# Kernel tuning notes

Measured on AMD Instinct MI355X. Metric: run time of the kernel, lower is better.

Reference implementation:

```python
import jax, jax.numpy as jnp
import numpy as np

EMB = 1024
HEAD = 64

def setup_inputs() -> dict:
    key = jax.random.key(0)
    k1, k2, k3, k4, k5 = jax.random.split(key, 5)
    x = jax.random.normal(k1, (4, 4096, EMB), dtype=jnp.float32)
    # qkv linear: weight [3*HEAD, EMB] torch-style -> store as [EMB, 3*HEAD]
    W_qkv = jax.random.normal(k2, (EMB, 3 * HEAD), dtype=jnp.float32) * (1.0 / np.sqrt(EMB))
    b_qkv = jax.random.normal(k3, (3 * HEAD,), dtype=jnp.float32) * 0.01
    W_out = jax.random.normal(k4, (HEAD, EMB), dtype=jnp.float32) * (1.0 / np.sqrt(HEAD))
    b_out = jax.random.normal(k5, (EMB,), dtype=jnp.float32) * 0.01
    return {"x": x, "W_qkv": W_qkv, "b_qkv": b_qkv, "W_out": W_out, "b_out": b_out}

def reference(x, W_qkv, b_qkv, W_out, b_out):
    qkv = jnp.einsum('bse,ed->bsd', x, W_qkv) + b_qkv            # [B,S,3H]
    q, k, v = jnp.split(qkv, 3, axis=-1)                          # each [B,S,H]
    scale = 1.0 / jnp.sqrt(jnp.asarray(q.shape[-1], q.dtype))
    scores = jnp.einsum('bqh,bkh->bqk', q, k) * scale             # [B,S,S]
    attn = jax.nn.softmax(scores, axis=-1)
    ctx = jnp.einsum('bqk,bkh->bqh', attn, v)                     # [B,S,H]
    return jnp.einsum('bqh,he->bqe', ctx, W_out) + b_out          # [B,S,E]
```

## Files before the change

### kernel.cpp

```cpp
#include <hip/hip_runtime.h>
#include <hip/hip_bf16.h>


#define LD 72

typedef __attribute__((ext_vector_type(8))) short short8;
typedef __attribute__((ext_vector_type(4))) short short4v;
typedef __attribute__((ext_vector_type(4))) float floatx4;

#define MFMA(a, b, c) __builtin_amdgcn_mfma_f32_16x16x32_bf16((a), (b), (c), 0, 0, 0)

__device__ __forceinline__ unsigned short f2bf(float f) {
  union { float f; unsigned u; } c; c.f = f;
  unsigned u = c.u + 0x7fffu + ((c.u >> 16) & 1u);
  return (unsigned short)(u >> 16);
}
__device__ __forceinline__ float asf(unsigned u) {
  union { unsigned u; float f; } c; c.u = u; return c.f;
}

__global__ __launch_bounds__(256) void prep_kernel(
    const float* __restrict__ Wqkv, const float* __restrict__ Wout,
    unsigned short* __restrict__ WtQkv, unsigned short* __restrict__ WtOut) {
  int idx = blockIdx.x * 256 + threadIdx.x;
  if (idx < 192 * 1024) {
    int n = idx >> 10, k = idx & 1023;
    WtQkv[idx] = f2bf(Wqkv[k * 192 + n]);
  } else if (idx < 192 * 1024 + 1024 * 64) {
    int j = idx - 192 * 1024;
    int e = j >> 6, d = j & 63;
    WtOut[j] = f2bf(Wout[d * 1024 + e]);
  }
}

__global__ __launch_bounds__(256, 2) void qkv_kernel(
    const float* __restrict__ x, const unsigned short* __restrict__ WtQkv,
    const float* __restrict__ bqkv,
    unsigned short* __restrict__ Qg, unsigned short* __restrict__ Kg,
    unsigned short* __restrict__ Vtg) {
  __shared__ __align__(16) unsigned short eQ[32 * LD];
  __shared__ __align__(16) unsigned short eK[32 * LD];
  __shared__ __align__(16) unsigned short eV[64 * 40];

  const int tid = threadIdx.x;
  const int wave = tid >> 6, lane = tid & 63, quad = lane >> 4, l16 = lane & 15;
  const int row0 = blockIdx.x * 32;
  const int colbase = wave * 48;

  floatx4 acc[2][3];
#pragma unroll
  for (int rt = 0; rt < 2; rt++)
#pragma unroll
    for (int t = 0; t < 3; t++) acc[rt][t] = (floatx4)(0.0f);

  const float* pA0 = x + (size_t)(row0 + l16) * 1024 + quad * 8;
  const float* pA1 = pA0 + 16 * 1024;
  const unsigned short* pB[3];
#pragma unroll
  for (int t = 0; t < 3; t++)
    pB[t] = WtQkv + (size_t)(colbase + t * 16 + l16) * 1024 + quad * 8;

  float4 ax[2][2][2];
  uint4 bw[3][2];
#pragma unroll
  for (int kh = 0; kh < 2; kh++) {
    ax[0][kh][0] = *(const float4*)(pA0 + kh * 32);
    ax[0][kh][1] = *(const float4*)(pA0 + kh * 32 + 4);
    ax[1][kh][0] = *(const float4*)(pA1 + kh * 32);
    ax[1][kh][1] = *(const float4*)(pA1 + kh * 32 + 4);
  }
#pragma unroll
  for (int t = 0; t < 3; t++) {
    bw[t][0] = *(const uint4*)(pB[t]);
    bw[t][1] = *(const uint4*)(pB[t] + 32);
  }

  for (int kc = 0; kc < 16; kc++) {
    short8 af[2][2];
#pragma unroll
    for (int rt = 0; rt < 2; rt++)
#pragma unroll
      for (int kh = 0; kh < 2; kh++) {
        const float* f0 = (const float*)&ax[rt][kh][0];
        const float* f1 = (const float*)&ax[rt][kh][1];
        short8 a;
        a[0] = (short)f2bf(f0[0]); a[1] = (short)f2bf(f0[1]);
        a[2] = (short)f2bf(f0[2]); a[3] = (short)f2bf(f0[3]);
        a[4] = (short)f2bf(f1[0]); a[5] = (short)f2bf(f1[1]);
        a[6] = (short)f2bf(f1[2]); a[7] = (short)f2bf(f1[3]);
        af[rt][kh] = a;
      }
    if (kc < 15) {
#pragma unroll
      for (int kh = 0; kh < 2; kh++) {
        ax[0][kh][0] = *(const float4*)(pA0 + 64 + kh * 32);
        ax[0][kh][1] = *(const float4*)(pA0 + 64 + kh * 32 + 4);
        ax[1][kh][0] = *(const float4*)(pA1 + 64 + kh * 32);
        ax[1][kh][1] = *(const float4*)(pA1 + 64 + kh * 32 + 4);
      }
    }
#pragma unroll
    for (int t = 0; t < 3; t++) {
      short8 b0 = __builtin_bit_cast(short8, bw[t][0]);
      short8 b1 = __builtin_bit_cast(short8, bw[t][1]);
      if (kc < 15) {
        bw[t][0] = *(const uint4*)(pB[t] + 64);
        bw[t][1] = *(const uint4*)(pB[t] + 96);
      }
#pragma unroll
      for (int rt = 0; rt < 2; rt++) {
        acc[rt][t] = MFMA(af[rt][0], b0, acc[rt][t]);
        acc[rt][t] = MFMA(af[rt][1], b1, acc[rt][t]);
      }
    }
    pA0 += 64; pA1 += 64;
#pragma unroll
    for (int t = 0; t < 3; t++) pB[t] += 64;
  }

  const int b = row0 >> 12, srow = row0 & 4095;
#pragma unroll
  for (int rt = 0; rt < 2; rt++)
#pragma unroll
    for (int t = 0; t < 3; t++) {
      int col = colbase + t * 16 + l16;
      float bias = bqkv[col];
      int sec = col >> 6, d = col & 63;
#pragma unroll
      for (int r = 0; r < 4; r++) {
        int lrow = rt * 16 + quad * 4 + r;
        float v = acc[rt][t][r] + bias;
        if (sec == 0)      eQ[lrow * LD + d] = f2bf(v * 0.125f);
        else if (sec == 1) eK[lrow * LD + d] = f2bf(v);
        else               eV[d * 40 + lrow] = f2bf(v);
      }
    }
  __syncthreads();
  {
    int r = tid >> 3, sg = tid & 7;
    *(uint4*)(Qg + (size_t)(row0 + r) * 64 + sg * 8) = *(const uint4*)(&eQ[r * LD + sg * 8]);
    *(uint4*)(Kg + (size_t)(row0 + r) * 64 + sg * 8) = *(const uint4*)(&eK[r * LD + sg * 8]);
    int tile = tid >> 7, rem = tid & 127, d = rem >> 1, half = rem & 1;
    *(uint4*)(Vtg + (((size_t)b * 256 + (srow >> 4) + tile) * 64 + d) * 16 + half * 8)
        = *(const uint4*)(&eV[d * 40 + tile * 16 + half * 8]);
  }
}

__global__ __launch_bounds__(256, 4) void attn_kernel(
    const unsigned short* __restrict__ Qg, const unsigned short* __restrict__ Kg,
    const unsigned short* __restrict__ Vtg,
    unsigned short* __restrict__ Opart, float* __restrict__ Lpart) {
  __shared__ __align__(16) unsigned short Ks[64 * LD];
  __shared__ __align__(16) unsigned short Vs[64 * LD];
  __shared__ __align__(16) unsigned short QP[64 * LD];

  const int tid = threadIdx.x;
  const int wave = tid >> 6, lane = tid & 63, quad = lane >> 4, l16 = lane & 15;
  const int bid = blockIdx.x;
  const int combo = bid & 15, qt = bid >> 4;
  const int b = combo >> 2, split = combo & 3;
  const int q0 = qt * 64, key0 = split * 1024;

  {
    int r = tid >> 2, seg = tid & 3;
    const uint4* s = (const uint4*)(Qg + ((size_t)b * 4096 + q0 + r) * 64 + seg * 16);
    *(uint4*)(&QP[r * LD + seg * 16])     = s[0];
    *(uint4*)(&QP[r * LD + seg * 16 + 8]) = s[1];
  }
  short8 aq0 = *(const short8*)(&QP[(wave * 16 + l16) * LD + quad * 8]);
  short8 aq1 = *(const short8*)(&QP[(wave * 16 + l16) * LD + 32 + quad * 8]);

  floatx4 o[4];
  float lsum[4];
#pragma unroll
  for (int t = 0; t < 4; t++) o[t] = (floatx4)(0.0f);
#pragma unroll
  for (int r = 0; r < 4; r++) lsum[r] = 0.0f;

  const int kr = tid >> 2, kseg = tid & 3;
  const unsigned short* Kbase = Kg + ((size_t)b * 4096 + key0) * 64;
  const unsigned short* Vt0 = Vtg + ((size_t)b * 256 + (key0 >> 4)) * 1024;

  uint4 pk0, pk1, pv0, pv1;
  pk0 = *(const uint4*)(Kbase + (size_t)kr * 64 + kseg * 16);
  pk1 = *(const uint4*)(Kbase + (size_t)kr * 64 + kseg * 16 + 8);
  pv0 = *(const uint4*)(Vt0 + ((size_t)kseg * 64 + kr) * 16);
  pv1 = *(const uint4*)(Vt0 + ((size_t)kseg * 64 + kr) * 16 + 8);

  unsigned short* Pw = &QP[wave * 16 * LD];

  for (int kc = 0; kc < 16; kc++) {
    __syncthreads();
    *(uint4*)(&Ks[kr * LD + kseg * 16])     = pk0;
    *(uint4*)(&Ks[kr * LD + kseg * 16 + 8]) = pk1;
    *(uint4*)(&Vs[kr * LD + kseg * 16])     = pv0;
    *(uint4*)(&Vs[kr * LD + kseg * 16 + 8]) = pv1;
    __syncthreads();
    if (kc < 15) {
      int nk = (kc + 1) * 64;
      int tl = (kc + 1) * 4 + kseg;
      pk0 = *(const uint4*)(Kbase + (size_t)(nk + kr) * 64 + kseg * 16);
      pk1 = *(const uint4*)(Kbase + (size_t)(nk + kr) * 64 + kseg * 16 + 8);
      pv0 = *(const uint4*)(Vt0 + ((size_t)tl * 64 + kr) * 16);
      pv1 = *(const uint4*)(Vt0 + ((size_t)tl * 64 + kr) * 16 + 8);
    }

    floatx4 sc[4];
#pragma unroll
    for (int t = 0; t < 4; t++) sc[t] = (floatx4)(0.0f);
#pragma unroll
    for (int t = 0; t < 4; t++) {
      short8 b0 = *(const short8*)(&Ks[(t * 16 + l16) * LD + quad * 8]);
      short8 b1 = *(const short8*)(&Ks[(t * 16 + l16) * LD + 32 + quad * 8]);
      sc[t] = MFMA(aq0, b0, sc[t]);
      sc[t] = MFMA(aq1, b1, sc[t]);
    }

#pragma unroll
    for (int r = 0; r < 4; r++) {
#pragma unroll
      for (int t = 0; t < 4; t++) {
        float pv = __expf(sc[t][r]);
        lsum[r] += pv;
        Pw[(quad * 4 + r) * LD + t * 16 + l16] = f2bf(pv);
      }
    }
    short8 ap0 = *(const short8*)(&Pw[l16 * LD + quad * 8]);
    short8 ap1 = *(const short8*)(&Pw[l16 * LD + 32 + quad * 8]);
#pragma unroll
    for (int t = 0; t < 4; t++) {
      short8 b0 = *(const short8*)(&Vs[(t * 16 + l16) * LD + quad * 8]);
      short8 b1 = *(const short8*)(&Vs[(t * 16 + l16) * LD + 32 + quad * 8]);
      o[t] = MFMA(ap0, b0, o[t]);
      o[t] = MFMA(ap1, b1, o[t]);
    }
  }

#pragma unroll
  for (int r = 0; r < 4; r++) {
#pragma unroll
    for (int off = 1; off < 16; off <<= 1) lsum[r] += __shfl_xor(lsum[r], off, 64);
  }

  unsigned short* Ob = Opart + ((size_t)bid * 64 + wave * 16) * 64;
#pragma unroll
  for (int t = 0; t < 4; t++)
#pragma unroll
    for (int r = 0; r < 4; r++)
      Ob[(quad * 4 + r) * 64 + t * 16 + l16] = f2bf(o[t][r]);
  if (l16 == 0) {
#pragma unroll
    for (int r = 0; r < 4; r++)
      Lpart[bid * 64 + wave * 16 + quad * 4 + r] = lsum[r];
  }
}

__global__ __launch_bounds__(256, 4) void combine_kernel(
    const unsigned short* __restrict__ Opart, const float* __restrict__ Lpart,
    const unsigned short* __restrict__ WtOut, const float* __restrict__ bout,
    float* __restrict__ out) {
  __shared__ __align__(16) unsigned short Cs[4][16 * LD];
  __shared__ __align__(16) unsigned short Wl[128 * LD];

  const int tid = threadIdx.x;
  const int wave = tid >> 6, lane = tid & 63, quad = lane >> 4, l16 = lane & 15;
  const int cid = blockIdx.x;
  const int eq = cid & 3, qt = (cid >> 2) & 63, b = cid >> 8;
  const int e0 = eq * 256;

  const int q = lane >> 2, d0 = (lane & 3) * 16;
  float accv[16];
#pragma unroll
  for (int i = 0; i < 16; i++) accv[i] = 0.0f;
  float lq = 0.0f;
#pragma unroll
  for (int s = 0; s < 4; s++) {
    int pid = qt * 16 + b * 4 + s;
    const unsigned short* src = Opart + ((size_t)pid * 64 + wave * 16 + q) * 64 + d0;
    uint4 h0 = *(const uint4*)src;
    uint4 h1 = *(const uint4*)(src + 8);
    const unsigned* hw = (const unsigned*)&h0;
#pragma unroll
    for (int i = 0; i < 4; i++) {
      accv[2 * i]     += asf(hw[i] << 16);
      accv[2 * i + 1] += asf(hw[i] & 0xFFFF0000u);
    }
    const unsigned* hw1 = (const unsigned*)&h1;
#pragma unroll
    for (int i = 0; i < 4; i++) {
      accv[8 + 2 * i]     += asf(hw1[i] << 16);
      accv[8 + 2 * i + 1] += asf(hw1[i] & 0xFFFF0000u);
    }
    lq += Lpart[pid * 64 + wave * 16 + q];
  }
  float inv = 1.0f / lq;
  short8 c0, c1;
#pragma unroll
  for (int i = 0; i < 8; i++) {
    c0[i] = (short)f2bf(accv[i] * inv);
    c1[i] = (short)f2bf(accv[8 + i] * inv);
  }
  *(short8*)(&Cs[wave][q * LD + d0])     = c0;
  *(short8*)(&Cs[wave][q * LD + d0 + 8]) = c1;
  short8 ao0 = *(const short8*)(&Cs[wave][l16 * LD + quad * 8]);
  short8 ao1 = *(const short8*)(&Cs[wave][l16 * LD + 32 + quad * 8]);

  const size_t orow0 = (size_t)b * 4096 + qt * 64 + wave * 16;
#pragma unroll 1
  for (int ec = 0; ec < 2; ec++) {
    int ebase = e0 + ec * 128;
    __syncthreads();
    {
      int er = tid >> 1, half = tid & 1;
      const uint4* s = (const uint4*)(WtOut + (size_t)(ebase + er) * 64 + half * 32);
      uint4 w0 = s[0], w1 = s[1], w2 = s[2], w3 = s[3];
      *(uint4*)(&Wl[er * LD + half * 32])      = w0;
      *(uint4*)(&Wl[er * LD + half * 32 + 8])  = w1;
      *(uint4*)(&Wl[er * LD + half * 32 + 16]) = w2;
      *(uint4*)(&Wl[er * LD + half * 32 + 24]) = w3;
    }
    __syncthreads();
    floatx4 a2[8];
#pragma unroll
    for (int t = 0; t < 8; t++) a2[t] = (floatx4)(0.0f);
#pragma unroll
    for (int t = 0; t < 8; t++) {
      short8 b0 = *(const short8*)(&Wl[(t * 16 + l16) * LD + quad * 8]);
      short8 b1 = *(const short8*)(&Wl[(t * 16 + l16) * LD + 32 + quad * 8]);
      a2[t] = MFMA(ao0, b0, a2[t]);
      a2[t] = MFMA(ao1, b1, a2[t]);
    }
#pragma unroll
    for (int t = 0; t < 8; t++) {
      int e = ebase + t * 16 + l16;
      float bo = bout[e];
#pragma unroll
      for (int r = 0; r < 4; r++)
        out[(orow0 + quad * 4 + r) * 1024 + e] = a2[t][r] + bo;
    }
  }
}

extern "C" void kernel_launch(void* const* d_in, const int* in_sizes, int n_in,
                              void* d_out, int out_size, void* d_ws, size_t ws_size,
                              hipStream_t stream) {
  const float* x    = (const float*)d_in[0];
  const float* Wqkv = (const float*)d_in[1];
  const float* bqkv = (const float*)d_in[2];
  const float* Wout = (const float*)d_in[3];
  const float* bout = (const float*)d_in[4];
  float* out = (float*)d_out;

  unsigned short* ws = (unsigned short*)d_ws;
  unsigned short* Qg    = ws;
  unsigned short* Kg    = Qg + 1048576;
  unsigned short* Vtg   = Kg + 1048576;
  unsigned short* WtQkv = Vtg + 1048576;
  unsigned short* WtOut = WtQkv + 196608;
  unsigned short* Opart = WtOut + 65536;
  float*          Lpart = (float*)(Opart + 4194304);

  prep_kernel<<<1024, 256, 0, stream>>>(Wqkv, Wout, WtQkv, WtOut);
  qkv_kernel<<<512, 256, 0, stream>>>(x, WtQkv, bqkv, Qg, Kg, Vtg);
  attn_kernel<<<1024, 256, 0, stream>>>(Qg, Kg, Vtg, Opart, Lpart);
  combine_kernel<<<1024, 256, 0, stream>>>(Opart, Lpart, WtOut, bout, out);
}
```

Baseline: 208.5 us.

## Stage QKV projection tiles through double-buffered LDS instead of per-wave global loads

Reworks the QKV projection GEMM so each block cooperatively loads its x tile (converted to bf16 once) and the full 192-column weight slice into double-buffered shared memory, then feeds MFMAs from LDS. Previously every wave re-read and re-converted x rows, and each wave loaded its weight columns straight from global memory. Each x element is now converted once per block instead of once per wave, and global traffic is coalesced across the block. In exchange the kernel uses much more LDS (about 60KB), adds a barrier per k-step, and reuses the staging buffers for the epilogue, which may limit occupancy below the 2-blocks launch bound.

```diff
diff --git a/kernel.cpp b/kernel.cpp
--- a/kernel.cpp
+++ b/kernel.cpp
@@ -38,9 +38,8 @@
     const float* __restrict__ bqkv,
     unsigned short* __restrict__ Qg, unsigned short* __restrict__ Kg,
     unsigned short* __restrict__ Vtg) {
-  __shared__ __align__(16) unsigned short eQ[32 * LD];
-  __shared__ __align__(16) unsigned short eK[32 * LD];
-  __shared__ __align__(16) unsigned short eV[64 * 40];
+  __shared__ __align__(16) unsigned short XS[2][32 * LD];
+  __shared__ __align__(16) unsigned short WS[2][192 * LD];
 
   const int tid = threadIdx.x;
   const int wave = tid >> 6, lane = tid & 63, quad = lane >> 4, l16 = lane & 15;
@@ -53,71 +52,70 @@
 #pragma unroll
     for (int t = 0; t < 3; t++) acc[rt][t] = (floatx4)(0.0f);
 
-  const float* pA0 = x + (size_t)(row0 + l16) * 1024 + quad * 8;
-  const float* pA1 = pA0 + 16 * 1024;
-  const unsigned short* pB[3];
-#pragma unroll
-  for (int t = 0; t < 3; t++)
-    pB[t] = WtQkv + (size_t)(colbase + t * 16 + l16) * 1024 + quad * 8;
-
-  float4 ax[2][2][2];
-  uint4 bw[3][2];
-#pragma unroll
-  for (int kh = 0; kh < 2; kh++) {
-    ax[0][kh][0] = *(const float4*)(pA0 + kh * 32);
-    ax[0][kh][1] = *(const float4*)(pA0 + kh * 32 + 4);
-    ax[1][kh][0] = *(const float4*)(pA1 + kh * 32);
-    ax[1][kh][1] = *(const float4*)(pA1 + kh * 32 + 4);
-  }
-#pragma unroll
-  for (int t = 0; t < 3; t++) {
-    bw[t][0] = *(const uint4*)(pB[t]);
-    bw[t][1] = *(const uint4*)(pB[t] + 32);
-  }
+  const int xr = tid >> 3, xj = tid & 7;
+  const float* gx = x + (size_t)(row0 + xr) * 1024 + xj * 8;
+  const unsigned short* gw = WtQkv + (size_t)xr * 1024 + xj * 8;
+
+  {
+    float4 xa = *(const float4*)(gx);
+    float4 xb = *(const float4*)(gx + 4);
+    uint4 wv[6];
+#pragma unroll
+    for (int i = 0; i < 6; i++) wv[i] = *(const uint4*)(gw + i * 32768);
+    short8 xc;
+    xc[0] = (short)f2bf(xa.x); xc[1] = (short)f2bf(xa.y);
+    xc[2] = (short)f2bf(xa.z); xc[3] = (short)f2bf(xa.w);
+    xc[4] = (short)f2bf(xb.x); xc[5] = (short)f2bf(xb.y);
+    xc[6] = (short)f2bf(xb.z); xc[7] = (short)f2bf(xb.w);
+    *(short8*)(&XS[0][xr * LD + xj * 8]) = xc;
+#pragma unroll
+    for (int i = 0; i < 6; i++)
+      *(uint4*)(&WS[0][(xr + 32 * i) * LD + xj * 8]) = wv[i];
+  }
+  __syncthreads();
 
   for (int kc = 0; kc < 16; kc++) {
-    short8 af[2][2];
-#pragma unroll
-    for (int rt = 0; rt < 2; rt++)
-#pragma unroll
-      for (int kh = 0; kh < 2; kh++) {
-        const float* f0 = (const float*)&ax[rt][kh][0];
-        const float* f1 = (const float*)&ax[rt][kh][1];
-        short8 a;
-        a[0] = (short)f2bf(f0[0]); a[1] = (short)f2bf(f0[1]);
-        a[2] = (short)f2bf(f0[2]); a[3] = (short)f2bf(f0[3]);
-        a[4] = (short)f2bf(f1[0]); a[5] = (short)f2bf(f1[1]);
-        a[6] = (short)f2bf(f1[2]); a[7] = (short)f2bf(f1[3]);
-        af[rt][kh] = a;
-      }
+    const int buf = kc & 1;
+    float4 nxa, nxb;
+    uint4 nwv[6];
     if (kc < 15) {
-#pragma unroll
-      for (int kh = 0; kh < 2; kh++) {
-        ax[0][kh][0] = *(const float4*)(pA0 + 64 + kh * 32);
-        ax[0][kh][1] = *(const float4*)(pA0 + 64 + kh * 32 + 4);
-        ax[1][kh][0] = *(const float4*)(pA1 + 64 + kh * 32);
-        ax[1][kh][1] = *(const float4*)(pA1 + 64 + kh * 32 + 4);
-      }
-    }
+      const float* gxn = gx + (kc + 1) * 64;
+      nxa = *(const float4*)(gxn);
+      nxb = *(const float4*)(gxn + 4);
+      const unsigned short* gwn = gw + (kc + 1) * 64;
+#pragma unroll
+      for (int i = 0; i < 6; i++) nwv[i] = *(const uint4*)(gwn + i * 32768);
+    }
+    short8 a0 = *(const short8*)(&XS[buf][l16 * LD + quad * 8]);
+    short8 a0h = *(const short8*)(&XS[buf][l16 * LD + 32 + quad * 8]);
+    short8 a1 = *(const short8*)(&XS[buf][(16 + l16) * LD + quad * 8]);
+    short8 a1h = *(const short8*)(&XS[buf][(16 + l16) * LD + 32 + quad * 8]);
 #pragma unroll
     for (int t = 0; t < 3; t++) {
-      short8 b0 = __builtin_bit_cast(short8, bw[t][0]);
-      short8 b1 = __builtin_bit_cast(short8, bw[t][1]);
-      if (kc < 15) {
-        bw[t][0] = *(const uint4*)(pB[t] + 64);
-        bw[t][1] = *(const uint4*)(pB[t] + 96);
-      }
-#pragma unroll
-      for (int rt = 0; rt < 2; rt++) {
-        acc[rt][t] = MFMA(af[rt][0], b0, acc[rt][t]);
-        acc[rt][t] = MFMA(af[rt][1], b1, acc[rt][t]);
-      }
-    }
-    pA0 += 64; pA1 += 64;
-#pragma unroll
-    for (int t = 0; t < 3; t++) pB[t] += 64;
-  }
-
+      short8 b0 = *(const short8*)(&WS[buf][(colbase + t * 16 + l16) * LD + quad * 8]);
+      short8 b1 = *(const short8*)(&WS[buf][(colbase + t * 16 + l16) * LD + 32 + quad * 8]);
+      acc[0][t] = MFMA(a0, b0, acc[0][t]);
+      acc[0][t] = MFMA(a0h, b1, acc[0][t]);
+      acc[1][t] = MFMA(a1, b0, acc[1][t]);
+      acc[1][t] = MFMA(a1h, b1, acc[1][t]);
+    }
+    if (kc < 15) {
+      short8 xc;
+      xc[0] = (short)f2bf(nxa.x); xc[1] = (short)f2bf(nxa.y);
+      xc[2] = (short)f2bf(nxa.z); xc[3] = (short)f2bf(nxa.w);
+      xc[4] = (short)f2bf(nxb.x); xc[5] = (short)f2bf(nxb.y);
+      xc[6] = (short)f2bf(nxb.z); xc[7] = (short)f2bf(nxb.w);
+      *(short8*)(&XS[buf ^ 1][xr * LD + xj * 8]) = xc;
+#pragma unroll
+      for (int i = 0; i < 6; i++)
+        *(uint4*)(&WS[buf ^ 1][(xr + 32 * i) * LD + xj * 8]) = nwv[i];
+    }
+    __syncthreads();
+  }
+
+  unsigned short* eQ = &XS[0][0];
+  unsigned short* eK = &XS[1][0];
+  unsigned short* eV = &WS[0][0];
   const int b = row0 >> 12, srow = row0 & 4095;
 #pragma unroll
   for (int rt = 0; rt < 2; rt++)
```

After: 184.4 us. 11.5% less time.
